# Kernel tuning notes

Hardware: AMD Instinct MI355X
Metric: run time of the kernel (lower is better)

Reference implementation:

```python
import jax, jax.numpy as jnp
import numpy as np

B, N, C = 4, 2048, 1024
H = 16
D = C // H  # head_dim = 64
SCALE = 1.0 / np.sqrt(D).astype(np.float32)


def setup_inputs() -> dict:
    key = jax.random.key(0)
    ks = jax.random.split(key, 6)
    s = 0.02
    return {
        "x": jax.random.normal(ks[0], (B, N, C), dtype=jnp.float32),
        "Wq": jax.random.normal(ks[1], (C, C), dtype=jnp.float32) * s,
        "Wk": jax.random.normal(ks[2], (C, C), dtype=jnp.float32) * s,
        "Wv": jax.random.normal(ks[3], (C, C), dtype=jnp.float32) * s,
        "Wo": jax.random.normal(ks[4], (C, C), dtype=jnp.float32) * s,
        "bo": jax.random.normal(ks[5], (C,), dtype=jnp.float32) * s,
    }


def reference(x, Wq, Wk, Wv, Wo, bo):
    # q/k/v projections (no bias, qkv_bias=False), split heads -> [B,H,N,D]
    def heads(t):
        return t.reshape(B, N, H, D).transpose(0, 2, 1, 3)
    q = heads(x @ Wq)
    k = heads(x @ Wk)
    v = heads(x @ Wv)
    attn = jnp.einsum("bhnd,bhmd->bhnm", q, k) * SCALE  # [B,H,N,N]
    attn = jax.nn.softmax(attn, axis=-1)
    out = jnp.einsum("bhnm,bhmd->bhnd", attn, v)  # [B,H,N,D]
    out = out.transpose(0, 2, 1, 3).reshape(B, N, C)
    return out @ Wo + bo
```

## Files before the change

kernel.cpp:

```cpp
#include <hip/hip_runtime.h>
#include <hip/hip_bf16.h>


typedef __bf16 bf16x8 __attribute__((ext_vector_type(8)));
typedef __bf16 bf16x4 __attribute__((ext_vector_type(4)));
typedef float  f32x4  __attribute__((ext_vector_type(4)));
typedef unsigned int u32x4 __attribute__((ext_vector_type(4)));

#define LSCALE 0.18033688f

__device__ __forceinline__ f32x4 mfma16(bf16x8 a, bf16x8 b, f32x4 c) {
    return __builtin_amdgcn_mfma_f32_16x16x32_bf16(a, b, c, 0, 0, 0);
}

__device__ __forceinline__ unsigned short f2bf(float f) {
    unsigned u = __builtin_bit_cast(unsigned, f);
    u += 0x7fffu + ((u >> 16) & 1u);
    return (unsigned short)(u >> 16);
}

__device__ __forceinline__ unsigned cvt_pk_bf16(float lo, float hi) {
    unsigned r;
    asm("v_cvt_pk_bf16_f32 %0, %1, %2" : "=v"(r) : "v"(lo), "v"(hi));
    return r;
}

__device__ __forceinline__ bf16x4 trread(unsigned addr) {
    bf16x4 d;
    asm volatile("ds_read_b64_tr_b16 %0, %1" : "=v"(d) : "v"(addr));
    return d;
}

__device__ __forceinline__ void gload16(const ushort* g, ushort* l) {
    __builtin_amdgcn_global_load_lds(
        (const __attribute__((address_space(1))) void*)g,
        (__attribute__((address_space(3))) void*)l, 16, 0, 0);
}

__global__ void cast_bf16_kernel(const float4* __restrict__ in,
                                 ushort4* __restrict__ out, int n4) {
    int i = blockIdx.x * blockDim.x + threadIdx.x;
    if (i < n4) {
        float4 f = in[i];
        ushort4 r;
        r.x = f2bf(f.x); r.y = f2bf(f.y); r.z = f2bf(f.z); r.w = f2bf(f.w);
        out[i] = r;
    }
}

__global__ void transpose_cast_kernel(const float* __restrict__ Wq,
                                      const float* __restrict__ Wk,
                                      const float* __restrict__ Wv,
                                      const float* __restrict__ Wo,
                                      ushort* __restrict__ out) {
    __shared__ float tile[32][33];
    const int z = blockIdx.z;
    const float* W = (z == 0) ? Wq : (z == 1) ? Wk : (z == 2) ? Wv : Wo;
    ushort* o = out + (size_t)z * 1024 * 1024;
    const int k0 = blockIdx.x * 32, n0 = blockIdx.y * 32;
    const int tx = threadIdx.x, ty = threadIdx.y;
#pragma unroll
    for (int i = 0; i < 4; i++)
        tile[ty + 8 * i][tx] = W[(size_t)(k0 + ty + 8 * i) * 1024 + n0 + tx];
    __syncthreads();
#pragma unroll
    for (int i = 0; i < 4; i++)
        o[(size_t)(n0 + ty + 8 * i) * 1024 + k0 + tx] = f2bf(tile[tx][ty + 8 * i]);
}

template <int MODE>
__global__ __launch_bounds__(256) void gemm128(const ushort* __restrict__ A,
                                               const ushort* __restrict__ Bt,
                                               ushort* __restrict__ outB,
                                               float* __restrict__ outF,
                                               const float* __restrict__ bias) {
    __shared__ ushort As[128 * 32];
    __shared__ ushort Bs[128 * 32];
    const int tid = threadIdx.x;
    const int lane = tid & 63;
    const int wid = tid >> 6;
    const int wm = wid >> 1, wn = wid & 1;
    const int m0 = blockIdx.x * 128;
    const int n0 = blockIdx.y * 128;
    if (MODE == 0) Bt += (size_t)blockIdx.z * (1024 * 1024);

    f32x4 acc[4][4] = {};

    for (int k0 = 0; k0 < 1024; k0 += 32) {
#pragma unroll
        for (int it = 0; it < 2; ++it) {
            int e = (it * 256 + tid) * 8;
            int r = e >> 5, c = e & 31;
            gload16(&A[(size_t)(m0 + r) * 1024 + k0 + c], &As[e]);
            gload16(&Bt[(size_t)(n0 + r) * 1024 + k0 + c], &Bs[e]);
        }
        __syncthreads();

        bf16x8 a[4], b[4];
#pragma unroll
        for (int i = 0; i < 4; i++) {
            a[i] = *(const bf16x8*)&As[(wm * 64 + i * 16 + (lane & 15)) * 32 + (lane >> 4) * 8];
            b[i] = *(const bf16x8*)&Bs[(wn * 64 + i * 16 + (lane & 15)) * 32 + (lane >> 4) * 8];
        }
#pragma unroll
        for (int i = 0; i < 4; i++)
#pragma unroll
            for (int j = 0; j < 4; j++)
                acc[i][j] = mfma16(a[i], b[j], acc[i][j]);
        __syncthreads();
    }

    const float scl = (MODE == 0 && blockIdx.z == 0) ? LSCALE : 1.0f;
#pragma unroll
    for (int i = 0; i < 4; i++) {
        int row_b = m0 + wm * 64 + i * 16 + ((lane >> 4) * 4);
#pragma unroll
        for (int j = 0; j < 4; j++) {
            int col = n0 + wn * 64 + j * 16 + (lane & 15);
#pragma unroll
            for (int r = 0; r < 4; r++) {
                int row = row_b + r;
                float v = acc[i][j][r] * scl;
                if (MODE == 0) {
                    ushort* o = outB + (size_t)blockIdx.z * (8192ull * 1024);
                    int b = row >> 11, n = row & 2047, h = col >> 6, d = col & 63;
                    o[((((size_t)(b * 16 + h)) * 2048 + n) << 6) + d] = f2bf(v);
                } else {
                    outF[(size_t)row * 1024 + col] = v + bias[col];
                }
            }
        }
    }
}

__global__ __launch_bounds__(256) void attn_kernel(const ushort* __restrict__ Q,
                                                   const ushort* __restrict__ K,
                                                   const ushort* __restrict__ V,
                                                   ushort* __restrict__ O) {
    __shared__ ushort Ks[2][64 * 64];
    __shared__ ushort Vs[2][64 * 64];
    __shared__ ushort Ps[4][2][1024];
    const int tid = threadIdx.x;
    const int lane = tid & 63;
    const int wid = tid >> 6;
    const int g = lane >> 4;
    const int q16 = lane & 15;
    const int bid = blockIdx.x;
    const int swz = (bid & 7) * 128 + (bid >> 3);
    const int bh = swz >> 4;
    const int qt = swz & 15;
    const size_t base = (size_t)bh * (2048 * 64);

    const int qr0 = qt * 128 + wid * 32 + q16;
    bf16x8 qf[2][2];
#pragma unroll
    for (int u = 0; u < 2; ++u)
#pragma unroll
        for (int ks = 0; ks < 2; ++ks)
            qf[u][ks] = *(const bf16x8*)&Q[base + (size_t)(qr0 + u * 16) * 64 + ks * 32 + g * 8];

    bf16x8 onesb;
#pragma unroll
    for (int i = 0; i < 8; i++) onesb[i] = (__bf16)1.0f;

    f32x4 o[2][4] = {};
    f32x4 lacc[2] = {};
    float m_run[2] = {-1e30f, -1e30f};

    const int kci0 = tid, kci1 = 256 + tid;
    const int kkey0 = kci0 >> 3, kd0 = (kci0 & 7) * 8;
    const int kkey1 = kci1 >> 3, kd1 = (kci1 & 7) * 8;
    const int kbyt0 = (kkey0 * 128 + kd0 * 2) ^ ((kkey0 & 7) << 4);
    const int kbyt1 = (kkey1 * 128 + kd1 * 2) ^ ((kkey1 & 7) << 4);
    const int vkey0 = (kci0 & 127) >> 1, vd0 = (kci0 >> 7) * 16 + (kci0 & 1) * 8;
    const int vkey1 = (kci1 & 127) >> 1, vd1 = (kci1 >> 7) * 16 + (kci1 & 1) * 8;

    char* const KsB0 = (char*)&Ks[0][0];
    ushort* const Vs0 = &Vs[0][0];
    const unsigned vb0 = (unsigned)(size_t)&Vs[0][0];

    {
        uint4 k0 = *(const uint4*)&K[base + (size_t)kkey0 * 64 + kd0];
        uint4 k1 = *(const uint4*)&K[base + (size_t)kkey1 * 64 + kd1];
        gload16(&V[base + (size_t)vkey0 * 64 + vd0], &Vs0[kci0 * 8]);
        gload16(&V[base + (size_t)vkey1 * 64 + vd1], &Vs0[kci1 * 8]);
        *(uint4*)(KsB0 + kbyt0) = k0;
        *(uint4*)(KsB0 + kbyt1) = k1;
    }
    __syncthreads();

    int cur = 0;
    for (int kt = 0; kt < 2048; kt += 64) {
        const int nxt = cur ^ 1;
        const bool more = (kt + 64) < 2048;
        char* const KsBc = KsB0 + cur * 8192;
        const unsigned vbc = vb0 + cur * 8192;

        uint4 kn0, kn1;
        if (more) {
            const size_t nb = base + (size_t)(kt + 64) * 64;
            gload16(&V[nb + (size_t)vkey0 * 64 + vd0], &Vs0[nxt * 4096 + kci0 * 8]);
            gload16(&V[nb + (size_t)vkey1 * 64 + vd1], &Vs0[nxt * 4096 + kci1 * 8]);
            kn0 = *(const uint4*)&K[nb + (size_t)kkey0 * 64 + kd0];
            kn1 = *(const uint4*)&K[nb + (size_t)kkey1 * 64 + kd1];
        }

        f32x4 s[2][4] = {};
#pragma unroll
        for (int kb = 0; kb < 4; ++kb) {
#pragma unroll
            for (int ks = 0; ks < 2; ++ks) {
                int key = kb * 16 + q16;
                int d0 = ks * 32 + g * 8;
                int byt = (key * 128 + d0 * 2) ^ ((key & 7) << 4);
                bf16x8 kf = *(const bf16x8*)(KsBc + byt);
                s[0][kb] = mfma16(kf, qf[0][ks], s[0][kb]);
                s[1][kb] = mfma16(kf, qf[1][ks], s[1][kb]);
            }
        }

        bf16x8 pa[2][2];
#pragma unroll
        for (int u = 0; u < 2; ++u) {
            float t[4][4];
#pragma unroll
            for (int kb = 0; kb < 4; ++kb)
#pragma unroll
                for (int r = 0; r < 4; ++r) t[kb][r] = s[u][kb][r];

            float mx = fmaxf(fmaxf(fmaxf(t[0][0], t[0][1]), fmaxf(t[0][2], t[0][3])),
                             fmaxf(fmaxf(t[1][0], t[1][1]), fmaxf(t[1][2], t[1][3])));
            mx = fmaxf(mx, fmaxf(fmaxf(fmaxf(t[2][0], t[2][1]), fmaxf(t[2][2], t[2][3])),
                                 fmaxf(fmaxf(t[3][0], t[3][1]), fmaxf(t[3][2], t[3][3]))));
            mx = fmaxf(mx, __shfl_xor(mx, 16));
            mx = fmaxf(mx, __shfl_xor(mx, 32));
            float mn = fmaxf(m_run[u], mx);
            float fr = __builtin_amdgcn_exp2f(m_run[u] - mn);
            m_run[u] = mn;

            unsigned w[4][2];
#pragma unroll
            for (int kb = 0; kb < 4; ++kb) {
                float p0 = __builtin_amdgcn_exp2f(t[kb][0] - mn);
                float p1 = __builtin_amdgcn_exp2f(t[kb][1] - mn);
                float p2 = __builtin_amdgcn_exp2f(t[kb][2] - mn);
                float p3 = __builtin_amdgcn_exp2f(t[kb][3] - mn);
                w[kb][0] = cvt_pk_bf16(p0, p1);
                w[kb][1] = cvt_pk_bf16(p2, p3);
            }

            char* PsB = (char*)Ps[wid][u];
            {
                u32x4 c0 = {w[0][0], w[0][1], w[2][0], w[2][1]};
                u32x4 c1 = {w[1][0], w[1][1], w[3][0], w[3][1]};
                *(u32x4*)(PsB + ((lane * 32 + 0)  ^ ((lane & 7) << 4))) = c0;
                *(u32x4*)(PsB + ((lane * 32 + 16) ^ ((lane & 7) << 4))) = c1;
            }
            asm volatile("" ::: "memory");
            __builtin_amdgcn_sched_barrier(0);
            int s1 = q16 + 32 * (g & 1);
            int ch = (g >> 1) * 16;
            u32x4 r1 = *(const u32x4*)(PsB + ((s1 * 32 + ch) ^ ((s1 & 7) << 4)));
            u32x4 r2 = *(const u32x4*)(PsB + (((s1 + 16) * 32 + ch) ^ (((s1 + 16) & 7) << 4)));
            asm volatile("" ::: "memory");
            {
                u32x4 p0 = {r1.x, r1.y, r2.x, r2.y};
                u32x4 p1 = {r1.z, r1.w, r2.z, r2.w};
                pa[u][0] = __builtin_bit_cast(bf16x8, p0);
                pa[u][1] = __builtin_bit_cast(bf16x8, p1);
            }

            float fro[4];
#pragma unroll
            for (int r = 0; r < 4; ++r) fro[r] = __shfl(fr, g * 4 + r);
#pragma unroll
            for (int cb = 0; cb < 4; ++cb)
#pragma unroll
                for (int r = 0; r < 4; ++r) o[u][cb][r] *= fro[r];
#pragma unroll
            for (int r = 0; r < 4; ++r) lacc[u][r] *= fro[r];

            lacc[u] = mfma16(pa[u][0], onesb, lacc[u]);
            lacc[u] = mfma16(pa[u][1], onesb, lacc[u]);
        }

        bf16x4 vlo[4][2], vhi[4][2];
#pragma unroll
        for (int cb = 0; cb < 4; ++cb)
#pragma unroll
            for (int ks = 0; ks < 2; ++ks) {
                unsigned a = vbc + cb * 2048 + (ks * 32 + g * 8) * 32 + q16 * 8;
                vlo[cb][ks] = trread(a);
                vhi[cb][ks] = trread(a + 128);
            }
        asm volatile("s_waitcnt lgkmcnt(0)" ::: "memory");
        __builtin_amdgcn_sched_barrier(0);
#pragma unroll
        for (int cb = 0; cb < 4; ++cb)
#pragma unroll
            for (int ks = 0; ks < 2; ++ks) {
                bf16x8 vf = __builtin_shufflevector(vlo[cb][ks], vhi[cb][ks],
                                                    0, 1, 2, 3, 4, 5, 6, 7);
                o[0][cb] = mfma16(pa[0][ks], vf, o[0][cb]);
                o[1][cb] = mfma16(pa[1][ks], vf, o[1][cb]);
            }

        if (more) {
            char* const KsBn = KsB0 + nxt * 8192;
            *(uint4*)(KsBn + kbyt0) = kn0;
            *(uint4*)(KsBn + kbyt1) = kn1;
        }
        __syncthreads();
        cur = nxt;
    }

    const int b = bh >> 4, h = bh & 15;
#pragma unroll
    for (int u = 0; u < 2; ++u) {
#pragma unroll
        for (int r = 0; r < 4; ++r) {
            float inv = 1.0f / lacc[u][r];
            int row = qt * 128 + wid * 32 + u * 16 + g * 4 + r;
#pragma unroll
            for (int cb = 0; cb < 4; ++cb) {
                int col = h * 64 + cb * 16 + q16;
                O[((size_t)(b * 2048 + row)) * 1024 + col] = f2bf(o[u][cb][r] * inv);
            }
        }
    }
}

extern "C" void kernel_launch(void* const* d_in, const int* in_sizes, int n_in,
                              void* d_out, int out_size, void* d_ws, size_t ws_size,
                              hipStream_t stream) {
    const float* x  = (const float*)d_in[0];
    const float* Wq = (const float*)d_in[1];
    const float* Wk = (const float*)d_in[2];
    const float* Wv = (const float*)d_in[3];
    const float* Wo = (const float*)d_in[4];
    const float* bo = (const float*)d_in[5];
    float* out = (float*)d_out;

    if (ws_size < (size_t)72 * 1024 * 1024) return;
    ushort* ws  = (ushort*)d_ws;
    ushort* xb  = ws;
    ushort* wt  = xb + (size_t)8 * 1024 * 1024;
    ushort* qkv = wt + (size_t)4 * 1024 * 1024;
    ushort* ao  = xb;

    cast_bf16_kernel<<<8192, 256, 0, stream>>>((const float4*)x, (ushort4*)xb,
                                               2 * 1024 * 1024);
    transpose_cast_kernel<<<dim3(32, 32, 4), dim3(32, 8), 0, stream>>>(Wq, Wk, Wv, Wo, wt);
    gemm128<0><<<dim3(64, 8, 3), 256, 0, stream>>>(xb, wt, qkv, nullptr, nullptr);
    attn_kernel<<<1024, 256, 0, stream>>>(
        qkv, qkv + (size_t)8 * 1024 * 1024, qkv + (size_t)16 * 1024 * 1024, ao);
    gemm128<1><<<dim3(64, 8, 1), 256, 0, stream>>>(ao, wt + (size_t)3 * 1024 * 1024,
                                                   nullptr, out, bo);
}
```

Baseline: 237.0 us.

## Switch attention to 32x32 MFMA, shuffle-based P layout, and deferred rescaling

```diff
diff --git a/kernel.cpp b/kernel.cpp
--- a/kernel.cpp
+++ b/kernel.cpp
@@ -5,12 +5,18 @@
 typedef __bf16 bf16x8 __attribute__((ext_vector_type(8)));
 typedef __bf16 bf16x4 __attribute__((ext_vector_type(4)));
 typedef float  f32x4  __attribute__((ext_vector_type(4)));
+typedef float  f32x16 __attribute__((ext_vector_type(16)));
 typedef unsigned int u32x4 __attribute__((ext_vector_type(4)));
 
 #define LSCALE 0.18033688f
+#define DEFER_THR 8.0f
 
 __device__ __forceinline__ f32x4 mfma16(bf16x8 a, bf16x8 b, f32x4 c) {
     return __builtin_amdgcn_mfma_f32_16x16x32_bf16(a, b, c, 0, 0, 0);
+}
+
+__device__ __forceinline__ f32x16 mfma32(bf16x8 a, bf16x8 b, f32x16 c) {
+    return __builtin_amdgcn_mfma_f32_32x32x16_bf16(a, b, c, 0, 0, 0);
 }
 
 __device__ __forceinline__ unsigned short f2bf(float f) {
@@ -139,33 +145,29 @@
                                                    ushort* __restrict__ O) {
     __shared__ ushort Ks[2][64 * 64];
     __shared__ ushort Vs[2][64 * 64];
-    __shared__ ushort Ps[4][2][1024];
     const int tid = threadIdx.x;
     const int lane = tid & 63;
     const int wid = tid >> 6;
-    const int g = lane >> 4;
-    const int q16 = lane & 15;
+    const int hi = lane >> 5;
+    const int q32 = lane & 31;
     const int bid = blockIdx.x;
     const int swz = (bid & 7) * 128 + (bid >> 3);
     const int bh = swz >> 4;
     const int qt = swz & 15;
     const size_t base = (size_t)bh * (2048 * 64);
 
-    const int qr0 = qt * 128 + wid * 32 + q16;
-    bf16x8 qf[2][2];
-#pragma unroll
-    for (int u = 0; u < 2; ++u)
-#pragma unroll
-        for (int ks = 0; ks < 2; ++ks)
-            qf[u][ks] = *(const bf16x8*)&Q[base + (size_t)(qr0 + u * 16) * 64 + ks * 32 + g * 8];
+    const int qr = qt * 128 + wid * 32 + q32;
+    bf16x8 qf[4];
+#pragma unroll
+    for (int dc = 0; dc < 4; ++dc)
+        qf[dc] = *(const bf16x8*)&Q[base + (size_t)qr * 64 + dc * 16 + hi * 8];
 
     bf16x8 onesb;
 #pragma unroll
     for (int i = 0; i < 8; i++) onesb[i] = (__bf16)1.0f;
 
-    f32x4 o[2][4] = {};
-    f32x4 lacc[2] = {};
-    float m_run[2] = {-1e30f, -1e30f};
+    f32x16 o0 = {}, o1 = {}, lacc = {};
+    float m_run = -1e30f;
 
     const int kci0 = tid, kci1 = 256 + tid;
     const int kkey0 = kci0 >> 3, kd0 = (kci0 & 7) * 8;
@@ -205,105 +207,99 @@
             kn1 = *(const uint4*)&K[nb + (size_t)kkey1 * 64 + kd1];
         }
 
-        f32x4 s[2][4] = {};
-#pragma unroll
-        for (int kb = 0; kb < 4; ++kb) {
-#pragma unroll
-            for (int ks = 0; ks < 2; ++ks) {
-                int key = kb * 16 + q16;
-                int d0 = ks * 32 + g * 8;
-                int byt = (key * 128 + d0 * 2) ^ ((key & 7) << 4);
-                bf16x8 kf = *(const bf16x8*)(KsBc + byt);
-                s[0][kb] = mfma16(kf, qf[0][ks], s[0][kb]);
-                s[1][kb] = mfma16(kf, qf[1][ks], s[1][kb]);
-            }
-        }
-
-        bf16x8 pa[2][2];
-#pragma unroll
-        for (int u = 0; u < 2; ++u) {
-            float t[4][4];
-#pragma unroll
-            for (int kb = 0; kb < 4; ++kb)
-#pragma unroll
-                for (int r = 0; r < 4; ++r) t[kb][r] = s[u][kb][r];
-
-            float mx = fmaxf(fmaxf(fmaxf(t[0][0], t[0][1]), fmaxf(t[0][2], t[0][3])),
-                             fmaxf(fmaxf(t[1][0], t[1][1]), fmaxf(t[1][2], t[1][3])));
-            mx = fmaxf(mx, fmaxf(fmaxf(fmaxf(t[2][0], t[2][1]), fmaxf(t[2][2], t[2][3])),
-                                 fmaxf(fmaxf(t[3][0], t[3][1]), fmaxf(t[3][2], t[3][3]))));
-            mx = fmaxf(mx, __shfl_xor(mx, 16));
-            mx = fmaxf(mx, __shfl_xor(mx, 32));
-            float mn = fmaxf(m_run[u], mx);
-            float fr = __builtin_amdgcn_exp2f(m_run[u] - mn);
-            m_run[u] = mn;
-
-            unsigned w[4][2];
-#pragma unroll
-            for (int kb = 0; kb < 4; ++kb) {
-                float p0 = __builtin_amdgcn_exp2f(t[kb][0] - mn);
-                float p1 = __builtin_amdgcn_exp2f(t[kb][1] - mn);
-                float p2 = __builtin_amdgcn_exp2f(t[kb][2] - mn);
-                float p3 = __builtin_amdgcn_exp2f(t[kb][3] - mn);
-                w[kb][0] = cvt_pk_bf16(p0, p1);
-                w[kb][1] = cvt_pk_bf16(p2, p3);
-            }
-
-            char* PsB = (char*)Ps[wid][u];
-            {
-                u32x4 c0 = {w[0][0], w[0][1], w[2][0], w[2][1]};
-                u32x4 c1 = {w[1][0], w[1][1], w[3][0], w[3][1]};
-                *(u32x4*)(PsB + ((lane * 32 + 0)  ^ ((lane & 7) << 4))) = c0;
-                *(u32x4*)(PsB + ((lane * 32 + 16) ^ ((lane & 7) << 4))) = c1;
-            }
-            asm volatile("" ::: "memory");
+        f32x16 s0 = {}, s1 = {};
+#pragma unroll
+        for (int dc = 0; dc < 4; ++dc) {
+            const int dby = (dc * 16 + hi * 8) * 2;
+            bf16x8 kf0 = *(const bf16x8*)(KsBc + ((q32 * 128 + dby) ^ ((q32 & 7) << 4)));
+            bf16x8 kf1 = *(const bf16x8*)(KsBc + (((32 + q32) * 128 + dby) ^ ((q32 & 7) << 4)));
+            s0 = mfma32(kf0, qf[dc], s0);
+            s1 = mfma32(kf1, qf[dc], s1);
+        }
+
+        float ma = fmaxf(fmaxf(s0[0], s0[1]), fmaxf(s0[2], s0[3]));
+        float mb = fmaxf(fmaxf(s0[4], s0[5]), fmaxf(s0[6], s0[7]));
+        float mc = fmaxf(fmaxf(s0[8], s0[9]), fmaxf(s0[10], s0[11]));
+        float md = fmaxf(fmaxf(s0[12], s0[13]), fmaxf(s0[14], s0[15]));
+        float me = fmaxf(fmaxf(s1[0], s1[1]), fmaxf(s1[2], s1[3]));
+        float mf = fmaxf(fmaxf(s1[4], s1[5]), fmaxf(s1[6], s1[7]));
+        float mg = fmaxf(fmaxf(s1[8], s1[9]), fmaxf(s1[10], s1[11]));
+        float mh = fmaxf(fmaxf(s1[12], s1[13]), fmaxf(s1[14], s1[15]));
+        float mx = fmaxf(fmaxf(fmaxf(ma, mb), fmaxf(mc, md)),
+                         fmaxf(fmaxf(me, mf), fmaxf(mg, mh)));
+        mx = fmaxf(mx, __shfl_xor(mx, 32));
+
+        if (!__all(mx <= m_run + DEFER_THR)) {
+            float mn2 = fmaxf(m_run, mx);
+            float fr = __builtin_amdgcn_exp2f(m_run - mn2);
+            m_run = mn2;
+#pragma unroll
+            for (int r = 0; r < 16; ++r) {
+                float f = __shfl(fr, (r & 3) + 8 * (r >> 2) + 4 * hi);
+                o0[r] *= f; o1[r] *= f; lacc[r] *= f;
+            }
+        }
+        const float mn = m_run;
+
+#pragma unroll
+        for (int t = 0; t < 2; ++t) {
+            const f32x16 sv = t ? s1 : s0;
+
+            bf16x4 vv[8];
+#pragma unroll
+            for (int h2 = 0; h2 < 2; ++h2) {
+                const int kb = t * 32 + h2 * 16 + hi * 8;
+#pragma unroll
+                for (int dt = 0; dt < 2; ++dt) {
+                    const int d = dt * 32 + q32;
+                    unsigned a = vbc + (d >> 4) * 2048 + kb * 32 + (d & 15) * 8;
+                    vv[h2 * 4 + dt * 2 + 0] = trread(a);
+                    vv[h2 * 4 + dt * 2 + 1] = trread(a + 128);
+                }
+            }
+
+            unsigned wA[2][2], wB[2][2];
+#pragma unroll
+            for (int h2 = 0; h2 < 2; ++h2) {
+                float p0 = __builtin_amdgcn_exp2f(sv[8 * h2 + 0] - mn);
+                float p1 = __builtin_amdgcn_exp2f(sv[8 * h2 + 1] - mn);
+                float p2 = __builtin_amdgcn_exp2f(sv[8 * h2 + 2] - mn);
+                float p3 = __builtin_amdgcn_exp2f(sv[8 * h2 + 3] - mn);
+                float p4 = __builtin_amdgcn_exp2f(sv[8 * h2 + 4] - mn);
+                float p5 = __builtin_amdgcn_exp2f(sv[8 * h2 + 5] - mn);
+                float p6 = __builtin_amdgcn_exp2f(sv[8 * h2 + 6] - mn);
+                float p7 = __builtin_amdgcn_exp2f(sv[8 * h2 + 7] - mn);
+                wA[h2][0] = cvt_pk_bf16(p0, p1);
+                wA[h2][1] = cvt_pk_bf16(p2, p3);
+                wB[h2][0] = cvt_pk_bf16(p4, p5);
+                wB[h2][1] = cvt_pk_bf16(p6, p7);
+            }
+
+            asm volatile("s_waitcnt lgkmcnt(0)" ::: "memory");
             __builtin_amdgcn_sched_barrier(0);
-            int s1 = q16 + 32 * (g & 1);
-            int ch = (g >> 1) * 16;
-            u32x4 r1 = *(const u32x4*)(PsB + ((s1 * 32 + ch) ^ ((s1 & 7) << 4)));
-            u32x4 r2 = *(const u32x4*)(PsB + (((s1 + 16) * 32 + ch) ^ (((s1 + 16) & 7) << 4)));
-            asm volatile("" ::: "memory");
-            {
-                u32x4 p0 = {r1.x, r1.y, r2.x, r2.y};
-                u32x4 p1 = {r1.z, r1.w, r2.z, r2.w};
-                pa[u][0] = __builtin_bit_cast(bf16x8, p0);
-                pa[u][1] = __builtin_bit_cast(bf16x8, p1);
-            }
-
-            float fro[4];
-#pragma unroll
-            for (int r = 0; r < 4; ++r) fro[r] = __shfl(fr, g * 4 + r);
-#pragma unroll
-            for (int cb = 0; cb < 4; ++cb)
-#pragma unroll
-                for (int r = 0; r < 4; ++r) o[u][cb][r] *= fro[r];
-#pragma unroll
-            for (int r = 0; r < 4; ++r) lacc[u][r] *= fro[r];
-
-            lacc[u] = mfma16(pa[u][0], onesb, lacc[u]);
-            lacc[u] = mfma16(pa[u][1], onesb, lacc[u]);
-        }
-
-        bf16x4 vlo[4][2], vhi[4][2];
-#pragma unroll
-        for (int cb = 0; cb < 4; ++cb)
-#pragma unroll
-            for (int ks = 0; ks < 2; ++ks) {
-                unsigned a = vbc + cb * 2048 + (ks * 32 + g * 8) * 32 + q16 * 8;
-                vlo[cb][ks] = trread(a);
-                vhi[cb][ks] = trread(a + 128);
-            }
-        asm volatile("s_waitcnt lgkmcnt(0)" ::: "memory");
-        __builtin_amdgcn_sched_barrier(0);
-#pragma unroll
-        for (int cb = 0; cb < 4; ++cb)
-#pragma unroll
-            for (int ks = 0; ks < 2; ++ks) {
-                bf16x8 vf = __builtin_shufflevector(vlo[cb][ks], vhi[cb][ks],
-                                                    0, 1, 2, 3, 4, 5, 6, 7);
-                o[0][cb] = mfma16(pa[0][ks], vf, o[0][cb]);
-                o[1][cb] = mfma16(pa[1][ks], vf, o[1][cb]);
-            }
+
+#pragma unroll
+            for (int h2 = 0; h2 < 2; ++h2) {
+                unsigned oA0 = __shfl_xor(wA[h2][0], 32);
+                unsigned oA1 = __shfl_xor(wA[h2][1], 32);
+                unsigned oB0 = __shfl_xor(wB[h2][0], 32);
+                unsigned oB1 = __shfl_xor(wB[h2][1], 32);
+                u32x4 pw;
+                pw.x = hi ? oB0 : wA[h2][0];
+                pw.y = hi ? oB1 : wA[h2][1];
+                pw.z = hi ? wB[h2][0] : oA0;
+                pw.w = hi ? wB[h2][1] : oA1;
+                bf16x8 pa = __builtin_bit_cast(bf16x8, pw);
+
+                lacc = mfma32(pa, onesb, lacc);
+                bf16x8 vf0 = __builtin_shufflevector(vv[h2 * 4 + 0], vv[h2 * 4 + 1],
+                                                     0, 1, 2, 3, 4, 5, 6, 7);
+                bf16x8 vf1 = __builtin_shufflevector(vv[h2 * 4 + 2], vv[h2 * 4 + 3],
+                                                     0, 1, 2, 3, 4, 5, 6, 7);
+                o0 = mfma32(pa, vf0, o0);
+                o1 = mfma32(pa, vf1, o1);
+            }
+        }
 
         if (more) {
             char* const KsBn = KsB0 + nxt * 8192;
@@ -316,17 +312,12 @@
 
     const int b = bh >> 4, h = bh & 15;
 #pragma unroll
-    for (int u = 0; u < 2; ++u) {
-#pragma unroll
-        for (int r = 0; r < 4; ++r) {
-            float inv = 1.0f / lacc[u][r];
-            int row = qt * 128 + wid * 32 + u * 16 + g * 4 + r;
-#pragma unroll
-            for (int cb = 0; cb < 4; ++cb) {
-                int col = h * 64 + cb * 16 + q16;
-                O[((size_t)(b * 2048 + row)) * 1024 + col] = f2bf(o[u][cb][r] * inv);
-            }
-        }
+    for (int r = 0; r < 16; ++r) {
+        float inv = 1.0f / lacc[r];
+        int row = qt * 128 + wid * 32 + (r & 3) + 8 * (r >> 2) + 4 * hi;
+        size_t rb = (size_t)(b * 2048 + row) * 1024 + h * 64;
+        O[rb + q32]      = f2bf(o0[r] * inv);
+        O[rb + 32 + q32] = f2bf(o1[r] * inv);
     }
 }
 
```

New measurement: 219.8 us. -7.2%, faster.
